# Kernel optimization log

Hardware: AMD Instinct MI355X
Metric: run time of the kernel (lower is better)

Reference implementation:

```python
import jax, jax.numpy as jnp
import numpy as np

N_V = 50000
N_E = 800000
IN = 128
OUT = 128
ADD_SELF_LOOPS = True


def setup_inputs() -> dict:
    key = jax.random.key(0)
    ks = jax.random.split(key, 7)
    x = jax.random.normal(ks[0], (N_V, IN), dtype=jnp.float32)
    # random edges, avoiding self-loops (src != dst) to match a simple graph
    src = jax.random.randint(ks[1], (N_E,), 0, N_V, dtype=jnp.int32)
    off = jax.random.randint(ks[2], (N_E,), 1, N_V, dtype=jnp.int32)
    dst = (src + off) % N_V
    edge_index = jnp.stack([src, dst], axis=0)  # [2, N_E]
    # edge_w_builder: Linear(2*IN, OUT) + Tanh   (torch default uniform init)
    s1 = 1.0 / float(np.sqrt(2 * IN))
    W_edge = jax.random.uniform(ks[3], (2 * IN, OUT), jnp.float32, -s1, s1)
    b_edge = jax.random.uniform(ks[4], (OUT,), jnp.float32, -s1, s1)
    # lin: Linear(IN, OUT, bias=False)
    s2 = 1.0 / float(np.sqrt(IN))
    W_lin = jax.random.uniform(ks[5], (IN, OUT), jnp.float32, -s2, s2)
    bias = jax.random.uniform(ks[6], (OUT,), jnp.float32, -s2, s2)
    return {"x": x, "edge_index": edge_index, "W_edge": W_edge,
            "b_edge": b_edge, "W_lin": W_lin, "bias": bias}


def reference(x, edge_index, W_edge, b_edge, W_lin, bias):
    # The sheaf construction uses indices (src*OUT+c, dst*OUT+c): strictly
    # channel-diagonal blocks. The Hadamard product L * (E + I) therefore
    # reduces per-edge-per-channel:
    #   off-diag (u,w in E0):  (-norm_uw) * s_ec
    #   diagonal (v,v):        (1 - 1/d_v) * 1   (self-loops added),
    # and solver = I - L*(E+I) gives
    #   off-diag: +norm_uw * s_ec,   diag: 1/d_v.
    src, dst = edge_index[0], edge_index[1]
    # edge MLP: tanh(Linear(cat(x_src, x_dst)))  -> [N_E, OUT]
    sheaf_w = jnp.tanh(jnp.concatenate([x[src], x[dst]], axis=1) @ W_edge + b_edge)
    # symmetric-normalized Laplacian weights over graph with self-loops
    deg = jax.ops.segment_sum(jnp.ones((N_E,), x.dtype), src, num_segments=N_V)
    if ADD_SELF_LOOPS:
        deg = deg + 1.0
    dinv = jnp.where(deg > 0, jax.lax.rsqrt(deg), 0.0)  # D^{-1/2}
    norm = dinv[src] * dinv[dst]                        # [N_E]
    x_lin = x @ W_lin                                   # [N_V, OUT]
    # out[v,c] = diag_v * x_lin[v,c] + sum_{e: src=v} norm_e * s_ec * x_lin[dst_e,c]
    msgs = (norm[:, None] * sheaf_w) * x_lin[dst]       # [N_E, OUT]
    agg = jax.ops.segment_sum(msgs, src, num_segments=N_V)
    diag = (dinv * dinv)[:, None] if ADD_SELF_LOOPS else jnp.zeros((N_V, 1), x.dtype)
    out = diag * x_lin + agg + bias
    return out, sheaf_w
```

## Files before the change

kernel.cpp:

```cpp
#include <hip/hip_runtime.h>
#include <hip/hip_bf16.h>

#define NV 50000
#define NE 800000
#define C  128
#define CAP 80

typedef __attribute__((ext_vector_type(8))) short short8;
typedef __attribute__((ext_vector_type(4))) float f32x4;

__device__ __forceinline__ float fast_tanh(float v) {
    float av = fabsf(v);
    float t  = __expf(-2.0f * av);
    float r  = (1.0f - t) / (1.0f + t);
    return copysignf(r, v);
}

__device__ __forceinline__ unsigned short f2bf(float f) {
    __hip_bfloat16 h = __float2bfloat16(f);
    return reinterpret_cast<unsigned short&>(h);
}
__device__ __forceinline__ float bflo(unsigned u) { return __uint_as_float(u << 16); }
__device__ __forceinline__ float bfhi(unsigned u) { return __uint_as_float(u & 0xffff0000u); }

__global__ __launch_bounds__(256) void k_zero(int* cur) {
    int v = blockIdx.x * 256 + threadIdx.x;
    if (v < NV) cur[v] = 0;
}

__global__ __launch_bounds__(256) void k_fillb(
    const int* __restrict__ src, const int* __restrict__ dst,
    int* cur, unsigned long long* __restrict__ bkt) {
    int e = blockIdx.x * 256 + threadIdx.x;
    if (e >= NE) return;
    int s = src[e];
    int p = atomicAdd(&cur[s], 1);
    if (p < CAP)
        bkt[(size_t)s * CAP + p] =
            ((unsigned long long)(unsigned)dst[e] << 32) | (unsigned)e;
}

__global__ __launch_bounds__(256) void k_dinv(const int* __restrict__ cur, float* dinv) {
    int v = blockIdx.x * 256 + threadIdx.x;
    if (v < NV) dinv[v] = rsqrtf((float)cur[v] + 1.0f);
}

__global__ __launch_bounds__(256) void k_cast_w(const float* __restrict__ We,
                                                const float* __restrict__ Wl,
                                                unsigned short* __restrict__ Wt) {
    int gid = blockIdx.x * 256 + threadIdx.x;
    if (gid >= 384 * 128) return;
    int n = gid >> 7, k = gid & 127;
    float v;
    if      (n < 128) v = We[(size_t)k * C + n];
    else if (n < 256) v = We[(size_t)(128 + k) * C + (n - 128)];
    else              v = Wl[(size_t)k * C + (n - 256)];
    Wt[(size_t)n * 128 + k] = f2bf(v);
}

__global__ __launch_bounds__(256) void gemm_mfma(
    const float* __restrict__ x, const unsigned short* __restrict__ Wt,
    const float* __restrict__ be,
    float* __restrict__ A, unsigned* __restrict__ BXu)
{
    __shared__ unsigned short xs[128 * 128];
    const int tid  = threadIdx.x;
    const int row0 = blockIdx.x * 128;

    #pragma unroll
    for (int i = 0; i < 8; ++i) {
        int L   = tid + i * 256;
        int row = L >> 4;
        int c   = L & 15;
        int grow = row0 + row;
        float4 f0 = make_float4(0.f,0.f,0.f,0.f), f1 = f0;
        if (grow < NV) {
            const float* p = x + (size_t)grow * C + c * 8;
            f0 = *(const float4*)p;
            f1 = *(const float4*)(p + 4);
        }
        unsigned short r[8];
        r[0]=f2bf(f0.x); r[1]=f2bf(f0.y); r[2]=f2bf(f0.z); r[3]=f2bf(f0.w);
        r[4]=f2bf(f1.x); r[5]=f2bf(f1.y); r[6]=f2bf(f1.z); r[7]=f2bf(f1.w);
        *(uint4*)(&xs[row * 128 + (c ^ (row & 7)) * 8]) = *(uint4*)r;
    }
    __syncthreads();

    const int w    = tid >> 6;
    const int lane = tid & 63;
    const int col  = lane & 15;
    const int kgrp = lane >> 4;

    for (int ct = 0; ct < 24; ++ct) {
        f32x4 acc[2];
        acc[0] = (f32x4){0.f, 0.f, 0.f, 0.f};
        acc[1] = (f32x4){0.f, 0.f, 0.f, 0.f};
        const int n = ct * 16 + col;
        #pragma unroll
        for (int kt = 0; kt < 4; ++kt) {
            const int k0 = kt * 32 + kgrp * 8;
            short8 b = *(const short8*)(Wt + (size_t)n * 128 + k0);
            #pragma unroll
            for (int rs = 0; rs < 2; ++rs) {
                int row = w * 32 + rs * 16 + col;
                int cc  = (k0 >> 3) ^ (row & 7);
                short8 a = *(const short8*)(&xs[row * 128 + cc * 8]);
                acc[rs] = __builtin_amdgcn_mfma_f32_16x16x32_bf16(a, b, acc[rs], 0, 0, 0);
            }
        }
        if (ct < 8) {
            const int nn = n;
            const float bv = be[nn];
            #pragma unroll
            for (int rs = 0; rs < 2; ++rs)
                #pragma unroll
                for (int r = 0; r < 4; ++r) {
                    int grow = row0 + w * 32 + rs * 16 + kgrp * 4 + r;
                    if (grow < NV) A[(size_t)grow * C + nn] = acc[rs][r] + bv;
                }
        } else {
            const int isXL = (ct >= 16) ? 1 : 0;
            const int nn   = n - (isXL ? 256 : 128);
            #pragma unroll
            for (int rs = 0; rs < 2; ++rs)
                #pragma unroll
                for (int r = 0; r < 4; ++r) {
                    float own  = acc[rs][r];
                    float part = __shfl_xor(own, 1);
                    if (!(lane & 1)) {
                        int grow = row0 + w * 32 + rs * 16 + kgrp * 4 + r;
                        if (grow < NV) {
                            unsigned pk = (unsigned)f2bf(own) |
                                          ((unsigned)f2bf(part) << 16);
                            BXu[((size_t)grow * 64 + (nn >> 1)) * 2 + isXL] = pk;
                        }
                    }
                }
        }
    }
}

__global__ __launch_bounds__(256) void k_gather(
    const int* __restrict__ cnt, const unsigned long long* __restrict__ bkt,
    const float* __restrict__ dinv, const float* __restrict__ A,
    const uint2* __restrict__ BX, const float* __restrict__ bias,
    float* __restrict__ out, float* __restrict__ sheaf)
{
    int v = blockIdx.x * 4 + (threadIdx.x >> 6);
    if (v >= NV) return;
    int lane = threadIdx.x & 63;

    float2* S2 = (float2*)sheaf;

    float  di = dinv[v];
    float2 a  = ((const float2*)A)[(size_t)v * 64 + lane];
    uint2  pv = BX[(size_t)v * 64 + lane];
    float2 b2 = ((const float2*)bias)[lane];
    float  dd = di * di;
    float accx = dd * bflo(pv.y) + b2.x;
    float accy = dd * bfhi(pv.y) + b2.y;

    int deg = cnt[v]; if (deg > CAP) deg = CAP;
    const unsigned long long* eb = bkt + (size_t)v * CAP;

    for (int base = 0; base < deg; base += 64) {
        int nb = deg - base; if (nb > 64) nb = 64;
        unsigned long long my = 0; float dn = 0.f;
        if (lane < nb) {
            my = eb[base + lane];
            dn = di * dinv[(int)(my >> 32)];
        }

        int j = 0;
        for (; j + 8 <= nb; j += 8) {
            unsigned long long pk[8];
            float nr[8];
            uint2 q[8];
            #pragma unroll
            for (int u = 0; u < 8; ++u) {
                pk[u] = __shfl(my, j + u);
                nr[u] = __shfl(dn, j + u);
            }
            #pragma unroll
            for (int u = 0; u < 8; ++u)
                q[u] = BX[(size_t)(int)(pk[u] >> 32) * 64 + lane];
            #pragma unroll
            for (int u = 0; u < 8; ++u) {
                float2 sv;
                sv.x = fast_tanh(a.x + bflo(q[u].x));
                sv.y = fast_tanh(a.y + bfhi(q[u].x));
                S2[(size_t)(unsigned)(pk[u] & 0xffffffffull) * 64 + lane] = sv;
                accx += nr[u] * sv.x * bflo(q[u].y);
                accy += nr[u] * sv.y * bfhi(q[u].y);
            }
        }
        for (; j < nb; ++j) {
            unsigned long long pk = __shfl(my, j);
            float nrm = __shfl(dn, j);
            int d = (int)(pk >> 32);
            uint2 q = BX[(size_t)d * 64 + lane];
            float2 sv;
            sv.x = fast_tanh(a.x + bflo(q.x));
            sv.y = fast_tanh(a.y + bfhi(q.x));
            S2[(size_t)(unsigned)(pk & 0xffffffffull) * 64 + lane] = sv;
            accx += nrm * sv.x * bflo(q.y);
            accy += nrm * sv.y * bfhi(q.y);
        }
    }
    float2 o; o.x = accx; o.y = accy;
    ((float2*)out)[(size_t)v * 64 + lane] = o;
}

extern "C" void kernel_launch(void* const* d_in, const int* in_sizes, int n_in,
                              void* d_out, int out_size, void* d_ws, size_t ws_size,
                              hipStream_t stream) {
    const float* x    = (const float*)d_in[0];
    const int*   ei   = (const int*)  d_in[1];
    const float* We   = (const float*)d_in[2];
    const float* be   = (const float*)d_in[3];
    const float* Wl   = (const float*)d_in[4];
    const float* bias = (const float*)d_in[5];

    float* out   = (float*)d_out;
    float* sheaf = out + (size_t)NV * C;

    const int* src = ei;
    const int* dst = ei + NE;

    char* wsb = (char*)d_ws;
    const size_t SEG = 256 * 1024;
    int*   cur  = (int*)(wsb);
    float* dinv = (float*)(wsb + SEG);
    unsigned long long* bkt = (unsigned long long*)(wsb + 2 * SEG);
    char*  after = wsb + 2 * SEG + (size_t)NV * CAP * 8;
    float* A  = (float*)after;
    uint2* BX = (uint2*)(A + (size_t)NV * C);
    unsigned short* Wt = (unsigned short*)(BX + (size_t)NV * 64);

    k_zero  <<<(NV + 255) / 256, 256, 0, stream>>>(cur);
    k_fillb <<<(NE + 255) / 256, 256, 0, stream>>>(src, dst, cur, bkt);
    k_dinv  <<<(NV + 255) / 256, 256, 0, stream>>>(cur, dinv);
    k_cast_w<<<(384 * 128 + 255) / 256, 256, 0, stream>>>(We, Wl, Wt);
    gemm_mfma<<<(NV + 127) / 128, 256, 0, stream>>>(x, Wt, be, A, (unsigned*)BX);
    k_gather<<<(NV + 3) / 4, 256, 0, stream>>>(cur, bkt, dinv, A, BX, bias, out, sheaf);
}
```

Measured before the change: 241.5 us.

## Merge prep kernels, pair BX stores, add nontemporal output stores and 4-wide tail

Merges the degree-normalisation and weight-cast kernels into one launch, saving one launch. In the GEMM, each BX column tile is computed together with its XL partner so both halves are written as a single 8-byte store instead of two strided 4-byte stores. The gather kernel now writes sheaf and out with nontemporal stores to avoid cache pollution, and gains a 4-wide unrolled remainder loop. The risks are more register pressure from the paired accumulators and possible store-coalescing differences with the nontemporal path.

```diff
diff --git a/kernel.cpp b/kernel.cpp
--- a/kernel.cpp
+++ b/kernel.cpp
@@ -5,6 +5,7 @@
 #define NE 800000
 #define C  128
 #define CAP 80
+#define NBV ((NV + 255) / 256)
 
 typedef __attribute__((ext_vector_type(8))) short short8;
 typedef __attribute__((ext_vector_type(4))) float f32x4;
@@ -22,6 +23,11 @@
 }
 __device__ __forceinline__ float bflo(unsigned u) { return __uint_as_float(u << 16); }
 __device__ __forceinline__ float bfhi(unsigned u) { return __uint_as_float(u & 0xffff0000u); }
+
+__device__ __forceinline__ void nt_store_f2(float2* p, float2 v) {
+    union { float2 f; unsigned long long u; } c; c.f = v;
+    __builtin_nontemporal_store(c.u, (unsigned long long*)p);
+}
 
 __global__ __launch_bounds__(256) void k_zero(int* cur) {
     int v = blockIdx.x * 256 + threadIdx.x;
@@ -40,28 +46,29 @@
             ((unsigned long long)(unsigned)dst[e] << 32) | (unsigned)e;
 }
 
-__global__ __launch_bounds__(256) void k_dinv(const int* __restrict__ cur, float* dinv) {
-    int v = blockIdx.x * 256 + threadIdx.x;
-    if (v < NV) dinv[v] = rsqrtf((float)cur[v] + 1.0f);
-}
-
-__global__ __launch_bounds__(256) void k_cast_w(const float* __restrict__ We,
-                                                const float* __restrict__ Wl,
-                                                unsigned short* __restrict__ Wt) {
-    int gid = blockIdx.x * 256 + threadIdx.x;
-    if (gid >= 384 * 128) return;
-    int n = gid >> 7, k = gid & 127;
-    float v;
-    if      (n < 128) v = We[(size_t)k * C + n];
-    else if (n < 256) v = We[(size_t)(128 + k) * C + (n - 128)];
-    else              v = Wl[(size_t)k * C + (n - 256)];
-    Wt[(size_t)n * 128 + k] = f2bf(v);
+__global__ __launch_bounds__(256) void k_prep(
+    const int* __restrict__ cur, float* __restrict__ dinv,
+    const float* __restrict__ We, const float* __restrict__ Wl,
+    unsigned short* __restrict__ Wt) {
+    if (blockIdx.x < NBV) {
+        int v = blockIdx.x * 256 + threadIdx.x;
+        if (v < NV) dinv[v] = rsqrtf((float)cur[v] + 1.0f);
+    } else {
+        int gid = (blockIdx.x - NBV) * 256 + threadIdx.x;
+        if (gid >= 384 * 128) return;
+        int n = gid >> 7, k = gid & 127;
+        float v;
+        if      (n < 128) v = We[(size_t)k * C + n];
+        else if (n < 256) v = We[(size_t)(128 + k) * C + (n - 128)];
+        else              v = Wl[(size_t)k * C + (n - 256)];
+        Wt[(size_t)n * 128 + k] = f2bf(v);
+    }
 }
 
 __global__ __launch_bounds__(256) void gemm_mfma(
     const float* __restrict__ x, const unsigned short* __restrict__ Wt,
     const float* __restrict__ be,
-    float* __restrict__ A, unsigned* __restrict__ BXu)
+    float* __restrict__ A, uint2* __restrict__ BX2)
 {
     __shared__ unsigned short xs[128 * 128];
     const int tid  = threadIdx.x;
@@ -91,8 +98,7 @@
     const int col  = lane & 15;
     const int kgrp = lane >> 4;
 
-    for (int ct = 0; ct < 24; ++ct) {
-        f32x4 acc[2];
+    auto compute_ct = [&](int ct, f32x4 acc[2]) {
         acc[0] = (f32x4){0.f, 0.f, 0.f, 0.f};
         acc[1] = (f32x4){0.f, 0.f, 0.f, 0.f};
         const int n = ct * 16 + col;
@@ -108,35 +114,43 @@
                 acc[rs] = __builtin_amdgcn_mfma_f32_16x16x32_bf16(a, b, acc[rs], 0, 0, 0);
             }
         }
-        if (ct < 8) {
-            const int nn = n;
-            const float bv = be[nn];
-            #pragma unroll
-            for (int rs = 0; rs < 2; ++rs)
-                #pragma unroll
-                for (int r = 0; r < 4; ++r) {
+    };
+
+    for (int ct = 0; ct < 8; ++ct) {
+        f32x4 acc[2];
+        compute_ct(ct, acc);
+        const int nn = ct * 16 + col;
+        const float bv = be[nn];
+        #pragma unroll
+        for (int rs = 0; rs < 2; ++rs)
+            #pragma unroll
+            for (int r = 0; r < 4; ++r) {
+                int grow = row0 + w * 32 + rs * 16 + kgrp * 4 + r;
+                if (grow < NV) A[(size_t)grow * C + nn] = acc[rs][r] + bv;
+            }
+    }
+
+    for (int p = 0; p < 8; ++p) {
+        f32x4 accb[2], accx[2];
+        compute_ct(8 + p,  accb);
+        compute_ct(16 + p, accx);
+        const int half = p * 8 + (col >> 1);
+        #pragma unroll
+        for (int rs = 0; rs < 2; ++rs)
+            #pragma unroll
+            for (int r = 0; r < 4; ++r) {
+                float ob = accb[rs][r], pb = __shfl_xor(ob, 1);
+                float ox = accx[rs][r], px = __shfl_xor(ox, 1);
+                if (!(lane & 1)) {
                     int grow = row0 + w * 32 + rs * 16 + kgrp * 4 + r;
-                    if (grow < NV) A[(size_t)grow * C + nn] = acc[rs][r] + bv;
-                }
-        } else {
-            const int isXL = (ct >= 16) ? 1 : 0;
-            const int nn   = n - (isXL ? 256 : 128);
-            #pragma unroll
-            for (int rs = 0; rs < 2; ++rs)
-                #pragma unroll
-                for (int r = 0; r < 4; ++r) {
-                    float own  = acc[rs][r];
-                    float part = __shfl_xor(own, 1);
-                    if (!(lane & 1)) {
-                        int grow = row0 + w * 32 + rs * 16 + kgrp * 4 + r;
-                        if (grow < NV) {
-                            unsigned pk = (unsigned)f2bf(own) |
-                                          ((unsigned)f2bf(part) << 16);
-                            BXu[((size_t)grow * 64 + (nn >> 1)) * 2 + isXL] = pk;
-                        }
+                    if (grow < NV) {
+                        uint2 pk;
+                        pk.x = (unsigned)f2bf(ob) | ((unsigned)f2bf(pb) << 16);
+                        pk.y = (unsigned)f2bf(ox) | ((unsigned)f2bf(px) << 16);
+                        BX2[(size_t)grow * 64 + half] = pk;
                     }
                 }
-        }
+            }
     }
 }
 
@@ -173,9 +187,7 @@
 
         int j = 0;
         for (; j + 8 <= nb; j += 8) {
-            unsigned long long pk[8];
-            float nr[8];
-            uint2 q[8];
+            unsigned long long pk[8]; float nr[8]; uint2 q[8];
             #pragma unroll
             for (int u = 0; u < 8; ++u) {
                 pk[u] = __shfl(my, j + u);
@@ -189,7 +201,27 @@
                 float2 sv;
                 sv.x = fast_tanh(a.x + bflo(q[u].x));
                 sv.y = fast_tanh(a.y + bfhi(q[u].x));
-                S2[(size_t)(unsigned)(pk[u] & 0xffffffffull) * 64 + lane] = sv;
+                nt_store_f2(&S2[(size_t)(unsigned)(pk[u] & 0xffffffffull) * 64 + lane], sv);
+                accx += nr[u] * sv.x * bflo(q[u].y);
+                accy += nr[u] * sv.y * bfhi(q[u].y);
+            }
+        }
+        for (; j + 4 <= nb; j += 4) {
+            unsigned long long pk[4]; float nr[4]; uint2 q[4];
+            #pragma unroll
+            for (int u = 0; u < 4; ++u) {
+                pk[u] = __shfl(my, j + u);
+                nr[u] = __shfl(dn, j + u);
+            }
+            #pragma unroll
+            for (int u = 0; u < 4; ++u)
+                q[u] = BX[(size_t)(int)(pk[u] >> 32) * 64 + lane];
+            #pragma unroll
+            for (int u = 0; u < 4; ++u) {
+                float2 sv;
+                sv.x = fast_tanh(a.x + bflo(q[u].x));
+                sv.y = fast_tanh(a.y + bfhi(q[u].x));
+                nt_store_f2(&S2[(size_t)(unsigned)(pk[u] & 0xffffffffull) * 64 + lane], sv);
                 accx += nr[u] * sv.x * bflo(q[u].y);
                 accy += nr[u] * sv.y * bfhi(q[u].y);
             }
@@ -202,13 +234,13 @@
             float2 sv;
             sv.x = fast_tanh(a.x + bflo(q.x));
             sv.y = fast_tanh(a.y + bfhi(q.x));
-            S2[(size_t)(unsigned)(pk & 0xffffffffull) * 64 + lane] = sv;
+            nt_store_f2(&S2[(size_t)(unsigned)(pk & 0xffffffffull) * 64 + lane], sv);
             accx += nrm * sv.x * bflo(q.y);
             accy += nrm * sv.y * bfhi(q.y);
         }
     }
     float2 o; o.x = accx; o.y = accy;
-    ((float2*)out)[(size_t)v * 64 + lane] = o;
+    nt_store_f2(&((float2*)out)[(size_t)v * 64 + lane], o);
 }
 
 extern "C" void kernel_launch(void* const* d_in, const int* in_sizes, int n_in,
@@ -239,8 +271,7 @@
 
     k_zero  <<<(NV + 255) / 256, 256, 0, stream>>>(cur);
     k_fillb <<<(NE + 255) / 256, 256, 0, stream>>>(src, dst, cur, bkt);
-    k_dinv  <<<(NV + 255) / 256, 256, 0, stream>>>(cur, dinv);
-    k_cast_w<<<(384 * 128 + 255) / 256, 256, 0, stream>>>(We, Wl, Wt);
-    gemm_mfma<<<(NV + 127) / 128, 256, 0, stream>>>(x, Wt, be, A, (unsigned*)BX);
+    k_prep  <<<NBV + (384 * 128 + 255) / 256, 256, 0, stream>>>(cur, dinv, We, Wl, Wt);
+    gemm_mfma<<<(NV + 127) / 128, 256, 0, stream>>>(x, Wt, be, A, BX);
     k_gather<<<(NV + 3) / 4, 256, 0, stream>>>(cur, bkt, dinv, A, BX, bias, out, sheaf);
 }
```

New measurement: 217.9 us. 1.11x faster.
